# Kernel tuning notes

Measured on AMD Instinct MI355X. Metric: run time of the kernel, lower is better.

## Reference

```python
import jax, jax.numpy as jnp
import numpy as np

C = 32
KSHAPE = (C, C, 3, 3)  # (C_out, C_in, kH, kW)
BN_EPS = 1e-5


def _binary_act(x):
    # forward: sign(x); backward: identity clipped to |x|<1 (STE)
    xc = jnp.clip(x, -1.0, 1.0)
    return jax.lax.stop_gradient(jnp.sign(x) - xc) + xc


def _binarize_weight(w_flat, shape):
    w = w_flat.reshape(shape)
    scale = jax.lax.stop_gradient(jnp.mean(jnp.abs(w)))  # global scalar scale, detached
    wc = jnp.clip(w, -1.0, 1.0)
    # forward: scale*sign(w); backward flows through clamp(w,-1,1)
    return jax.lax.stop_gradient(scale * jnp.sign(w) - wc) + wc


def _bi_conv_bn(x, w_flat, gamma, beta, stride):
    xb = _binary_act(x)
    w = _binarize_weight(w_flat, KSHAPE)
    y = jax.lax.conv_general_dilated(
        xb, w, window_strides=(stride, stride), padding=[(1, 1), (1, 1)],
        dimension_numbers=('NCHW', 'OIHW', 'NCHW'))
    # BatchNorm2d in training mode (batch stats, biased variance)
    m = jnp.mean(y, axis=(0, 2, 3), keepdims=True)
    v = jnp.mean((y - m) ** 2, axis=(0, 2, 3), keepdims=True)
    yhat = (y - m) * jax.lax.rsqrt(v + BN_EPS)
    return gamma.reshape(1, -1, 1, 1) * yhat + beta.reshape(1, -1, 1, 1)


def setup_inputs() -> dict:
    key = jax.random.key(0)
    k1, k2, k3 = jax.random.split(key, 3)
    return {
        'x': jax.random.normal(k1, (32, C, 160, 160), dtype=jnp.float32),
        'w1': jax.random.normal(k2, (C * C * 9, 1), dtype=jnp.float32) * 0.05,
        'gamma1': jnp.ones((C,), dtype=jnp.float32),
        'beta1': jnp.zeros((C,), dtype=jnp.float32),
        'w2': jax.random.normal(k3, (C * C * 9, 1), dtype=jnp.float32) * 0.05,
        'gamma2': jnp.ones((C,), dtype=jnp.float32),
        'beta2': jnp.zeros((C,), dtype=jnp.float32),
    }


def reference(x, w1, gamma1, beta1, w2, gamma2, beta2):
    # bireal residual block, stride=1 => skip_op is Identity
    inner = _bi_conv_bn(x, w1, gamma1, beta1, 1) + x
    out = _bi_conv_bn(inner, w2, gamma2, beta2, 1) + inner
    return out
```

## Files before the change

### kernel.cpp

```cpp
#include <hip/hip_runtime.h>
#include <stdint.h>

#define NIMG 32
#define CH 32
#define HH 160
#define WW 160
#define HWL (HH*WW)
#define PRS 164
#define PHH 162
#define PIMG (PHH*PRS)
#define NPIX (NIMG*HWL)
#define HALO_WORDS 968

#define OFF_P     0
#define OFF_P2    3400704
#define OFF_IT    (OFF_P2 + 3400704)
#define OFF_WP    (OFF_IT + 52428800)
#define OFF_CORR  (OFF_WP + 2304)
#define OFF_SC    (OFF_CORR + 2304)
#define OFF_SB    (OFF_SC + 128)

struct StatLine {
  int s1; int pad0; unsigned long long s2; char pad[112];
};

#define AS1 __attribute__((address_space(1)))
#define AS3 __attribute__((address_space(3)))
__device__ __forceinline__ void dma16(const void* g, void* l) {
  __builtin_amdgcn_global_load_lds((const AS1 void*)g, (AS3 void*)l, 16, 0, 0);
}

__device__ __forceinline__ unsigned short f2bf(float f) {
  unsigned u = __float_as_uint(f);
  u += 0x7fffu + ((u >> 16) & 1u);
  return (unsigned short)(u >> 16);
}
__device__ __forceinline__ float bf2f(unsigned short u) {
  return __uint_as_float((uint32_t)u << 16);
}

__device__ __forceinline__ void conv4(const uint32_t r[3][6], const uint32_t* wsh,
                                      int co, int& a0, int& a1, int& a2, int& a3)
{
  a0 = a1 = a2 = a3 = 0;
  #pragma unroll
  for (int dy = 0; dy < 3; ++dy) {
    #pragma unroll
    for (int dx = 0; dx < 3; ++dx) {
      uint32_t wvv = wsh[co * 9 + dy * 3 + dx];
      a0 += __popc(r[dy][0 + dx] ^ wvv);
      a1 += __popc(r[dy][1 + dx] ^ wvv);
      a2 += __popc(r[dy][2 + dx] ^ wvv);
      a3 += __popc(r[dy][3 + dx] ^ wvv);
    }
  }
}

__device__ __forceinline__ void bn_affine(const float* SCp, const StatLine* sb,
    const float* gamma, const float* beta, int c, float& A, float& B)
{
  double sc = (double)SCp[0];
  double m  = sc * (double)sb[c].s1 / (double)NPIX;
  double ms = sc * sc * (double)(long long)sb[c].s2 / (double)NPIX;
  float inv = (float)(1.0 / sqrt(ms - m * m + 1e-5));
  float gm = gamma[c];
  A = gm * inv * (float)sc;
  B = beta[c] - gm * inv * (float)m;
}

__global__ __launch_bounds__(256) void pack_prep(const float* __restrict__ x,
    const float* __restrict__ w1, const float* __restrict__ w2,
    uint32_t* __restrict__ P, uint32_t* __restrict__ P2, uint32_t* __restrict__ WP,
    int* __restrict__ CORR, float* __restrict__ SC, StatLine* __restrict__ SB)
{
  __shared__ float lds[8192];
  const int tid = threadIdx.x;
  const int b = blockIdx.x;

  if (b >= 3200) {
    if (b == 3442) {
      int* z = (int*)SB;
      for (int i = tid; i < 2048; i += 256) z[i] = 0;
      float* red = lds;
      uint32_t* wpl = (uint32_t*)(lds + 256);
      for (int cv = 0; cv < 2; ++cv) {
        const float* w = cv ? w2 : w1;
        float s = 0.f;
        #pragma unroll
        for (int j = 0; j < 9; ++j) {
          float4 v = *reinterpret_cast<const float4*>(w + (j * 256 + tid) * 4);
          s += fabsf(v.x) + fabsf(v.y) + fabsf(v.z) + fabsf(v.w);
        }
        red[tid] = s;
        __syncthreads();
        for (int st = 128; st > 0; st >>= 1) {
          if (tid < st) red[tid] += red[tid + st];
          __syncthreads();
        }
        if (tid == 0) SC[cv] = red[0] / 9216.0f;
        for (int i = tid; i < 288; i += 256) {
          int co = i / 9, t = i - co * 9;
          uint32_t bw = 0;
          for (int ci = 0; ci < 32; ++ci)
            bw |= (w[(co * 32 + ci) * 9 + t] > 0.0f) ? (1u << ci) : 0u;
          WP[cv * 288 + i] = bw;
          wpl[i] = bw;
        }
        __syncthreads();
        for (int i = tid; i < 288; i += 256) {
          int cls = i / 32, co = i - cls * 32;
          int hc = cls / 3, wc = cls - hc * 3;
          int corr = 0;
          for (int t = 0; t < 9; ++t) {
            int dy = t / 3 - 1, dx = t % 3 - 1;
            bool inval = (hc == 0 && dy == -1) || (hc == 2 && dy == 1) ||
                         (wc == 0 && dx == -1) || (wc == 2 && dx == 1);
            if (inval) corr += 32 - 2 * __popc(wpl[co * 9 + t]);
          }
          CORR[cv * 288 + cls * 32 + co] = corr;
        }
        __syncthreads();
      }
    } else {
      int k = (b - 3200) * 256 + tid;
      uint32_t* buf = (k < 32 * HALO_WORDS) ? P : P2;
      int j = k % (32 * HALO_WORDS);
      int img = j / HALO_WORDS;
      int r = j - img * HALO_WORDS;
      int pr, pc;
      if (r < 164)      { pr = 0;   pc = r; }
      else if (r < 328) { pr = 161; pc = r - 164; }
      else {
        int k2 = r - 328;
        pr = 1 + (k2 >> 2);
        int q = k2 & 3;
        pc = (q == 0) ? 0 : (160 + q);
      }
      buf[img * PIMG + pr * PRS + pc] = 0;
    }
    return;
  }

  int n = b / 100;
  int p0 = (b - n * 100) * 256;
  const float* xb = x + (size_t)n * CH * HWL + p0;
  #pragma unroll
  for (int it = 0; it < 8; ++it) {
    int c = it * 4 + (tid >> 6);
    dma16(xb + (size_t)c * HWL + (tid & 63) * 4, lds + c * 256);
  }
  __syncthreads();

  uint32_t bits = 0;
  #pragma unroll
  for (int c = 0; c < 32; ++c) {
    if (lds[c * 256 + tid] > 0.f) bits |= 1u << c;
  }
  int px = p0 + tid;
  int h = px / WW, w = px - h * WW;
  P[n * PIMG + (h + 1) * PRS + (w + 1)] = bits;
}

__global__ __launch_bounds__(256) void conv_stats(const uint32_t* __restrict__ P,
    const uint32_t* __restrict__ WP, const int* __restrict__ CORR,
    StatLine* __restrict__ sb)
{
  __shared__ uint32_t wsh[288];
  __shared__ int csh[288];
  __shared__ int ls1[32], ls2[32];
  const int tid = threadIdx.x;
  for (int i = tid; i < 288; i += 256) { wsh[i] = WP[i]; csh[i] = CORR[i]; }
  if (tid < 32) { ls1[tid] = 0; ls2[tid] = 0; }
  __syncthreads();

  int g = blockIdx.x * 256 + tid;
  int w4 = g % 40;
  int t1 = g / 40;
  int h = t1 % 160;
  int n = t1 / 160;

  const uint32_t* base = P + n * PIMG + h * PRS + w4 * 4;
  uint32_t r[3][6];
  #pragma unroll
  for (int dy = 0; dy < 3; ++dy) {
    uint4 a = *reinterpret_cast<const uint4*>(base + dy * PRS);
    uint2 bw = *reinterpret_cast<const uint2*>(base + dy * PRS + 4);
    r[dy][0] = a.x; r[dy][1] = a.y; r[dy][2] = a.z; r[dy][3] = a.w;
    r[dy][4] = bw.x; r[dy][5] = bw.y;
  }

  int rowc = (h == 0) ? 0 : ((h == 159) ? 6 : 3);
  int cls0  = rowc + ((w4 == 0) ? 0 : 1);
  int cls12 = rowc + 1;
  int cls3  = rowc + ((w4 == 39) ? 2 : 1);
  int lane = tid & 63;

  #pragma unroll
  for (int co = 0; co < 32; ++co) {
    int a0, a1, a2, a3;
    conv4(r, wsh, co, a0, a1, a2, a3);
    int d0 = 288 - 2 * a0 - csh[cls0 * 32 + co];
    int d1 = 288 - 2 * a1 - csh[cls12 * 32 + co];
    int d2 = 288 - 2 * a2 - csh[cls12 * 32 + co];
    int d3 = 288 - 2 * a3 - csh[cls3 * 32 + co];
    int ds = d0 + d1 + d2 + d3;
    int sq = d0 * d0 + d1 * d1 + d2 * d2 + d3 * d3;
    #pragma unroll
    for (int off = 32; off > 0; off >>= 1) {
      ds += __shfl_down(ds, off);
      sq += __shfl_down(sq, off);
    }
    if (lane == 0) { atomicAdd(&ls1[co], ds); atomicAdd(&ls2[co], sq); }
  }
  __syncthreads();
  if (tid < 32) {
    atomicAdd(&sb[tid].s1, ls1[tid]);
    atomicAdd(&sb[tid].s2, (unsigned long long)(long long)ls2[tid]);
  }
}

__global__ __launch_bounds__(256) void conv_bn1(const uint32_t* __restrict__ P,
    const uint32_t* __restrict__ WP, const int* __restrict__ CORR,
    const float* __restrict__ x, const float* __restrict__ SCp,
    const StatLine* __restrict__ sb, const float* __restrict__ gamma,
    const float* __restrict__ beta, unsigned short* __restrict__ IT,
    uint32_t* __restrict__ P2)
{
  __shared__ float xs[8192];
  __shared__ uint32_t wsh[288];
  __shared__ int csh[288];
  __shared__ float Ash[32], Bsh[32];
  const int tid = threadIdx.x;
  const int b = blockIdx.x;
  int n = b / 100;
  int p0 = (b - n * 100) * 256;
  const float* xb = x + (size_t)n * CH * HWL + p0;

  #pragma unroll
  for (int it = 0; it < 8; ++it) {
    int c = it * 4 + (tid >> 6);
    dma16(xb + (size_t)c * HWL + (tid & 63) * 4, xs + c * 256);
  }

  for (int i = tid; i < 288; i += 256) { wsh[i] = WP[i]; csh[i] = CORR[i]; }
  if (tid < 32) bn_affine(SCp, sb, gamma, beta, tid, Ash[tid], Bsh[tid]);

  int px = p0 + tid;
  int h = px / WW, w = px - h * WW;
  const uint32_t* bp = P + n * PIMG + h * PRS + w;
  uint32_t r9[3][3];
  #pragma unroll
  for (int dy = 0; dy < 3; ++dy) {
    r9[dy][0] = bp[dy * PRS + 0];
    r9[dy][1] = bp[dy * PRS + 1];
    r9[dy][2] = bp[dy * PRS + 2];
  }
  int hc = (h == 0) ? 0 : ((h == 159) ? 2 : 1);
  int wc = (w == 0) ? 0 : ((w == 159) ? 2 : 1);
  int cls = hc * 3 + wc;

  __syncthreads();

  uint32_t bits = 0;
  uint32_t ow[16];
  #pragma unroll
  for (int co = 0; co < 32; ++co) {
    int a = 0;
    #pragma unroll
    for (int dy = 0; dy < 3; ++dy) {
      #pragma unroll
      for (int dx = 0; dx < 3; ++dx)
        a += __popc(r9[dy][dx] ^ wsh[co * 9 + dy * 3 + dx]);
    }
    int d = 288 - 2 * a - csh[cls * 32 + co];
    float v = fmaf(Ash[co], (float)d, Bsh[co]) + xs[co * 256 + tid];
    if (v > 0.f) bits |= 1u << co;
    uint32_t bf = (uint32_t)f2bf(v);
    if ((co & 1) == 0) ow[co >> 1] = bf;
    else               ow[co >> 1] |= bf << 16;
  }
  P2[n * PIMG + (h + 1) * PRS + (w + 1)] = bits;
  uint4* ip = (uint4*)(IT + (size_t)(n * HWL + px) * 32);
  ip[0] = make_uint4(ow[0], ow[1], ow[2], ow[3]);
  ip[1] = make_uint4(ow[4], ow[5], ow[6], ow[7]);
  ip[2] = make_uint4(ow[8], ow[9], ow[10], ow[11]);
  ip[3] = make_uint4(ow[12], ow[13], ow[14], ow[15]);
}

__global__ __launch_bounds__(256, 2) void conv_bn2(const uint32_t* __restrict__ P2,
    const uint32_t* __restrict__ WP, const int* __restrict__ CORR,
    const unsigned short* __restrict__ IT, const float* __restrict__ SCp,
    const StatLine* __restrict__ sb, const float* __restrict__ gamma,
    const float* __restrict__ beta, float* __restrict__ out)
{
  __shared__ uint32_t wsh[288];
  __shared__ int csh[288];
  __shared__ float Ash[32], Bsh[32];
  const int tid = threadIdx.x;
  for (int i = tid; i < 288; i += 256) { wsh[i] = WP[i]; csh[i] = CORR[i]; }
  if (tid < 32) bn_affine(SCp, sb, gamma, beta, tid, Ash[tid], Bsh[tid]);
  __syncthreads();

  int g = blockIdx.x * 256 + tid;
  int w4 = g % 40;
  int t1 = g / 40;
  int h = t1 % 160;
  int n = t1 / 160;

  const uint32_t* base = P2 + n * PIMG + h * PRS + w4 * 4;
  uint32_t r[3][6];
  #pragma unroll
  for (int dy = 0; dy < 3; ++dy) {
    uint4 a = *reinterpret_cast<const uint4*>(base + dy * PRS);
    uint2 bw = *reinterpret_cast<const uint2*>(base + dy * PRS + 4);
    r[dy][0] = a.x; r[dy][1] = a.y; r[dy][2] = a.z; r[dy][3] = a.w;
    r[dy][4] = bw.x; r[dy][5] = bw.y;
  }
  int rowc = (h == 0) ? 0 : ((h == 159) ? 6 : 3);
  int cls0  = rowc + ((w4 == 0) ? 0 : 1);
  int cls12 = rowc + 1;
  int cls3  = rowc + ((w4 == 39) ? 2 : 1);

  int i = h * WW + w4 * 4;
  size_t pbase = (size_t)n * CH * HWL + i;

  uint4 tt[16];
  const uint4* ip = (const uint4*)(IT + (size_t)(n * HWL + i) * 32);
  #pragma unroll
  for (int q = 0; q < 16; ++q) tt[q] = ip[q];

  #pragma unroll
  for (int co = 0; co < 32; ++co) {
    int e0, e1, e2, e3;
    conv4(r, wsh, co, e0, e1, e2, e3);
    int f0 = 288 - 2 * e0 - csh[cls0 * 32 + co];
    int f1 = 288 - 2 * e1 - csh[cls12 * 32 + co];
    int f2 = 288 - 2 * e2 - csh[cls12 * 32 + co];
    int f3 = 288 - 2 * e3 - csh[cls3 * 32 + co];
    float A = Ash[co], Bv = Bsh[co];
    const int qw = co >> 3;
    const int ws = (co >> 1) & 3;
    const int hf = co & 1;
    uint32_t u0 = (ws == 0) ? tt[0 * 4 + qw].x : (ws == 1) ? tt[0 * 4 + qw].y
                : (ws == 2) ? tt[0 * 4 + qw].z : tt[0 * 4 + qw].w;
    uint32_t u1 = (ws == 0) ? tt[1 * 4 + qw].x : (ws == 1) ? tt[1 * 4 + qw].y
                : (ws == 2) ? tt[1 * 4 + qw].z : tt[1 * 4 + qw].w;
    uint32_t u2 = (ws == 0) ? tt[2 * 4 + qw].x : (ws == 1) ? tt[2 * 4 + qw].y
                : (ws == 2) ? tt[2 * 4 + qw].z : tt[2 * 4 + qw].w;
    uint32_t u3 = (ws == 0) ? tt[3 * 4 + qw].x : (ws == 1) ? tt[3 * 4 + qw].y
                : (ws == 2) ? tt[3 * 4 + qw].z : tt[3 * 4 + qw].w;
    float i0 = bf2f((unsigned short)(hf ? (u0 >> 16) : (u0 & 0xffff)));
    float i1 = bf2f((unsigned short)(hf ? (u1 >> 16) : (u1 & 0xffff)));
    float i2 = bf2f((unsigned short)(hf ? (u2 >> 16) : (u2 & 0xffff)));
    float i3 = bf2f((unsigned short)(hf ? (u3 >> 16) : (u3 & 0xffff)));
    float4 o;
    o.x = fmaf(A, (float)f0, Bv) + i0;
    o.y = fmaf(A, (float)f1, Bv) + i1;
    o.z = fmaf(A, (float)f2, Bv) + i2;
    o.w = fmaf(A, (float)f3, Bv) + i3;
    *reinterpret_cast<float4*>(out + pbase + (size_t)co * HWL) = o;
  }
}

extern "C" void kernel_launch(void* const* d_in, const int* in_sizes, int n_in,
                              void* d_out, int out_size, void* d_ws, size_t ws_size,
                              hipStream_t stream)
{
  (void)in_sizes; (void)n_in; (void)out_size; (void)ws_size;
  const float* x  = (const float*)d_in[0];
  const float* w1 = (const float*)d_in[1];
  const float* g1 = (const float*)d_in[2];
  const float* b1 = (const float*)d_in[3];
  const float* w2 = (const float*)d_in[4];
  const float* g2 = (const float*)d_in[5];
  const float* b2 = (const float*)d_in[6];
  float* out = (float*)d_out;
  char* ws = (char*)d_ws;

  uint32_t*       P    = (uint32_t*)(ws + OFF_P);
  uint32_t*       P2   = (uint32_t*)(ws + OFF_P2);
  unsigned short* IT   = (unsigned short*)(ws + OFF_IT);
  uint32_t*       WP   = (uint32_t*)(ws + OFF_WP);
  int*            CORR = (int*)(ws + OFF_CORR);
  float*          SC   = (float*)(ws + OFF_SC);
  StatLine*       SB   = (StatLine*)(ws + OFF_SB);

  pack_prep<<<3443, 256, 0, stream>>>(x, w1, w2, P, P2, WP, CORR, SC, SB);
  conv_stats<<<800, 256, 0, stream>>>(P, WP, CORR, SB);
  conv_bn1<<<3200, 256, 0, stream>>>(P, WP, CORR, x, SC, SB, g1, b1, IT, P2);
  conv_stats<<<800, 256, 0, stream>>>(P2, WP + 288, CORR + 288, SB + 32);
  conv_bn2<<<800, 256, 0, stream>>>(P2, WP + 288, CORR + 288, IT, SC + 1, SB + 32, g2, b2, out);
}
```

Baseline: 201.5 us.

## Store bf16 intermediate planar NCHW and stage it through LDS in conv_bn2

The bf16 residual intermediate moves from pixel-major (NHWC, 64B per pixel) to channel-planar NCHW layout. conv_bn1 now processes two pixels per thread with 512-pixel blocks, loading x in two 16-channel halves into LDS and writing coalesced ushort2 per channel. conv_bn2 DMA-loads the planar intermediate tile into LDS and computes two pixels per thread instead of four, with coalesced float2 output writes. The aim is to remove strided, poorly coalesced accesses and register-heavy unpacking, at the cost of extra barriers and a 32KB LDS tile that may limit occupancy.

Result: faster. 181.1 us (-10.1%).

```diff
diff --git a/kernel.cpp b/kernel.cpp
--- a/kernel.cpp
+++ b/kernel.cpp
@@ -14,8 +14,8 @@
 
 #define OFF_P     0
 #define OFF_P2    3400704
-#define OFF_IT    (OFF_P2 + 3400704)
-#define OFF_WP    (OFF_IT + 52428800)
+#define OFF_IN    (OFF_P2 + 3400704)
+#define OFF_WP    (OFF_IN + 52428800)
 #define OFF_CORR  (OFF_WP + 2304)
 #define OFF_SC    (OFF_CORR + 2304)
 #define OFF_SB    (OFF_SC + 128)
@@ -52,6 +52,21 @@
       a1 += __popc(r[dy][1 + dx] ^ wvv);
       a2 += __popc(r[dy][2 + dx] ^ wvv);
       a3 += __popc(r[dy][3 + dx] ^ wvv);
+    }
+  }
+}
+
+__device__ __forceinline__ void conv2(const uint32_t r[3][4], const uint32_t* wsh,
+                                      int co, int& a0, int& a1)
+{
+  a0 = a1 = 0;
+  #pragma unroll
+  for (int dy = 0; dy < 3; ++dy) {
+    #pragma unroll
+    for (int dx = 0; dx < 3; ++dx) {
+      uint32_t wvv = wsh[co * 9 + dy * 3 + dx];
+      a0 += __popc(r[dy][dx] ^ wvv);
+      a1 += __popc(r[dy][dx + 1] ^ wvv);
     }
   }
 }
@@ -223,7 +238,7 @@
     const uint32_t* __restrict__ WP, const int* __restrict__ CORR,
     const float* __restrict__ x, const float* __restrict__ SCp,
     const StatLine* __restrict__ sb, const float* __restrict__ gamma,
-    const float* __restrict__ beta, unsigned short* __restrict__ IT,
+    const float* __restrict__ beta, unsigned short* __restrict__ IN,
     uint32_t* __restrict__ P2)
 {
   __shared__ float xs[8192];
@@ -232,133 +247,133 @@
   __shared__ float Ash[32], Bsh[32];
   const int tid = threadIdx.x;
   const int b = blockIdx.x;
-  int n = b / 100;
-  int p0 = (b - n * 100) * 256;
+  int n = b / 50;
+  int p0 = (b - n * 50) * 512;
   const float* xb = x + (size_t)n * CH * HWL + p0;
 
   #pragma unroll
   for (int it = 0; it < 8; ++it) {
-    int c = it * 4 + (tid >> 6);
-    dma16(xb + (size_t)c * HWL + (tid & 63) * 4, xs + c * 256);
-  }
-
+    int q = it * 4 + (tid >> 6);
+    int c = q >> 1, hf = q & 1;
+    dma16(xb + (size_t)c * HWL + hf * 256 + (tid & 63) * 4,
+          xs + c * 512 + hf * 256 + (tid & 63) * 4);
+  }
   for (int i = tid; i < 288; i += 256) { wsh[i] = WP[i]; csh[i] = CORR[i]; }
   if (tid < 32) bn_affine(SCp, sb, gamma, beta, tid, Ash[tid], Bsh[tid]);
 
-  int px = p0 + tid;
-  int h = px / WW, w = px - h * WW;
-  const uint32_t* bp = P + n * PIMG + h * PRS + w;
-  uint32_t r9[3][3];
+  int p = p0 + 2 * tid;
+  int h = p / WW, wloc = p - h * WW;
+  const uint32_t* bp = P + n * PIMG + h * PRS + wloc;
+  uint32_t r[3][4];
   #pragma unroll
   for (int dy = 0; dy < 3; ++dy) {
-    r9[dy][0] = bp[dy * PRS + 0];
-    r9[dy][1] = bp[dy * PRS + 1];
-    r9[dy][2] = bp[dy * PRS + 2];
-  }
-  int hc = (h == 0) ? 0 : ((h == 159) ? 2 : 1);
-  int wc = (w == 0) ? 0 : ((w == 159) ? 2 : 1);
-  int cls = hc * 3 + wc;
-
-  __syncthreads();
-
-  uint32_t bits = 0;
-  uint32_t ow[16];
-  #pragma unroll
-  for (int co = 0; co < 32; ++co) {
-    int a = 0;
-    #pragma unroll
-    for (int dy = 0; dy < 3; ++dy) {
-      #pragma unroll
-      for (int dx = 0; dx < 3; ++dx)
-        a += __popc(r9[dy][dx] ^ wsh[co * 9 + dy * 3 + dx]);
-    }
-    int d = 288 - 2 * a - csh[cls * 32 + co];
-    float v = fmaf(Ash[co], (float)d, Bsh[co]) + xs[co * 256 + tid];
-    if (v > 0.f) bits |= 1u << co;
-    uint32_t bf = (uint32_t)f2bf(v);
-    if ((co & 1) == 0) ow[co >> 1] = bf;
-    else               ow[co >> 1] |= bf << 16;
-  }
-  P2[n * PIMG + (h + 1) * PRS + (w + 1)] = bits;
-  uint4* ip = (uint4*)(IT + (size_t)(n * HWL + px) * 32);
-  ip[0] = make_uint4(ow[0], ow[1], ow[2], ow[3]);
-  ip[1] = make_uint4(ow[4], ow[5], ow[6], ow[7]);
-  ip[2] = make_uint4(ow[8], ow[9], ow[10], ow[11]);
-  ip[3] = make_uint4(ow[12], ow[13], ow[14], ow[15]);
-}
-
-__global__ __launch_bounds__(256, 2) void conv_bn2(const uint32_t* __restrict__ P2,
+    uint2 u0 = *reinterpret_cast<const uint2*>(bp + dy * PRS);
+    uint2 u1 = *reinterpret_cast<const uint2*>(bp + dy * PRS + 2);
+    r[dy][0] = u0.x; r[dy][1] = u0.y; r[dy][2] = u1.x; r[dy][3] = u1.y;
+  }
+  int rowc = (h == 0) ? 0 : ((h == 159) ? 6 : 3);
+  int cls0 = rowc + ((wloc == 0) ? 0 : 1);
+  int cls1 = rowc + ((wloc == 158) ? 2 : 1);
+  size_t ibase = (size_t)n * CH * HWL + p;
+
+  __syncthreads();
+
+  uint32_t bb0 = 0, bb1 = 0;
+  #pragma unroll
+  for (int co = 0; co < 16; ++co) {
+    int a0, a1;
+    conv2(r, wsh, co, a0, a1);
+    int d0 = 288 - 2 * a0 - csh[cls0 * 32 + co];
+    int d1 = 288 - 2 * a1 - csh[cls1 * 32 + co];
+    float2 xv = *reinterpret_cast<const float2*>(xs + co * 512 + 2 * tid);
+    float v0 = fmaf(Ash[co], (float)d0, Bsh[co]) + xv.x;
+    float v1 = fmaf(Ash[co], (float)d1, Bsh[co]) + xv.y;
+    ushort2 o; o.x = f2bf(v0); o.y = f2bf(v1);
+    *reinterpret_cast<ushort2*>(IN + ibase + (size_t)co * HWL) = o;
+    if (v0 > 0.f) bb0 |= 1u << co;
+    if (v1 > 0.f) bb1 |= 1u << co;
+  }
+  __syncthreads();
+
+  #pragma unroll
+  for (int it = 0; it < 8; ++it) {
+    int q = it * 4 + (tid >> 6);
+    int c = q >> 1, hf = q & 1;
+    dma16(xb + (size_t)(16 + c) * HWL + hf * 256 + (tid & 63) * 4,
+          xs + c * 512 + hf * 256 + (tid & 63) * 4);
+  }
+  __syncthreads();
+
+  #pragma unroll
+  for (int co = 16; co < 32; ++co) {
+    int a0, a1;
+    conv2(r, wsh, co, a0, a1);
+    int d0 = 288 - 2 * a0 - csh[cls0 * 32 + co];
+    int d1 = 288 - 2 * a1 - csh[cls1 * 32 + co];
+    float2 xv = *reinterpret_cast<const float2*>(xs + (co - 16) * 512 + 2 * tid);
+    float v0 = fmaf(Ash[co], (float)d0, Bsh[co]) + xv.x;
+    float v1 = fmaf(Ash[co], (float)d1, Bsh[co]) + xv.y;
+    ushort2 o; o.x = f2bf(v0); o.y = f2bf(v1);
+    *reinterpret_cast<ushort2*>(IN + ibase + (size_t)co * HWL) = o;
+    if (v0 > 0.f) bb0 |= 1u << co;
+    if (v1 > 0.f) bb1 |= 1u << co;
+  }
+  uint32_t* pw = P2 + n * PIMG + (h + 1) * PRS + (wloc + 1);
+  pw[0] = bb0; pw[1] = bb1;
+}
+
+__global__ __launch_bounds__(256) void conv_bn2(const uint32_t* __restrict__ P2,
     const uint32_t* __restrict__ WP, const int* __restrict__ CORR,
-    const unsigned short* __restrict__ IT, const float* __restrict__ SCp,
+    const unsigned short* __restrict__ IN, const float* __restrict__ SCp,
     const StatLine* __restrict__ sb, const float* __restrict__ gamma,
     const float* __restrict__ beta, float* __restrict__ out)
 {
+  __shared__ unsigned short is[16384];
   __shared__ uint32_t wsh[288];
   __shared__ int csh[288];
   __shared__ float Ash[32], Bsh[32];
   const int tid = threadIdx.x;
+  const int b = blockIdx.x;
+  int n = b / 50;
+  int p0 = (b - n * 50) * 512;
+  const unsigned short* ib = IN + (size_t)n * CH * HWL + p0;
+
+  #pragma unroll
+  for (int it = 0; it < 8; ++it) {
+    int c = it * 4 + (tid >> 6);
+    dma16(ib + (size_t)c * HWL + (tid & 63) * 8, is + c * 512 + (tid & 63) * 8);
+  }
   for (int i = tid; i < 288; i += 256) { wsh[i] = WP[i]; csh[i] = CORR[i]; }
   if (tid < 32) bn_affine(SCp, sb, gamma, beta, tid, Ash[tid], Bsh[tid]);
-  __syncthreads();
-
-  int g = blockIdx.x * 256 + tid;
-  int w4 = g % 40;
-  int t1 = g / 40;
-  int h = t1 % 160;
-  int n = t1 / 160;
-
-  const uint32_t* base = P2 + n * PIMG + h * PRS + w4 * 4;
-  uint32_t r[3][6];
+
+  int p = p0 + 2 * tid;
+  int h = p / WW, wloc = p - h * WW;
+  const uint32_t* bp = P2 + n * PIMG + h * PRS + wloc;
+  uint32_t r[3][4];
   #pragma unroll
   for (int dy = 0; dy < 3; ++dy) {
-    uint4 a = *reinterpret_cast<const uint4*>(base + dy * PRS);
-    uint2 bw = *reinterpret_cast<const uint2*>(base + dy * PRS + 4);
-    r[dy][0] = a.x; r[dy][1] = a.y; r[dy][2] = a.z; r[dy][3] = a.w;
-    r[dy][4] = bw.x; r[dy][5] = bw.y;
+    uint2 u0 = *reinterpret_cast<const uint2*>(bp + dy * PRS);
+    uint2 u1 = *reinterpret_cast<const uint2*>(bp + dy * PRS + 2);
+    r[dy][0] = u0.x; r[dy][1] = u0.y; r[dy][2] = u1.x; r[dy][3] = u1.y;
   }
   int rowc = (h == 0) ? 0 : ((h == 159) ? 6 : 3);
-  int cls0  = rowc + ((w4 == 0) ? 0 : 1);
-  int cls12 = rowc + 1;
-  int cls3  = rowc + ((w4 == 39) ? 2 : 1);
-
-  int i = h * WW + w4 * 4;
-  size_t pbase = (size_t)n * CH * HWL + i;
-
-  uint4 tt[16];
-  const uint4* ip = (const uint4*)(IT + (size_t)(n * HWL + i) * 32);
-  #pragma unroll
-  for (int q = 0; q < 16; ++q) tt[q] = ip[q];
+  int cls0 = rowc + ((wloc == 0) ? 0 : 1);
+  int cls1 = rowc + ((wloc == 158) ? 2 : 1);
+  size_t obase = (size_t)n * CH * HWL + p;
+
+  __syncthreads();
 
   #pragma unroll
   for (int co = 0; co < 32; ++co) {
-    int e0, e1, e2, e3;
-    conv4(r, wsh, co, e0, e1, e2, e3);
-    int f0 = 288 - 2 * e0 - csh[cls0 * 32 + co];
-    int f1 = 288 - 2 * e1 - csh[cls12 * 32 + co];
-    int f2 = 288 - 2 * e2 - csh[cls12 * 32 + co];
-    int f3 = 288 - 2 * e3 - csh[cls3 * 32 + co];
-    float A = Ash[co], Bv = Bsh[co];
-    const int qw = co >> 3;
-    const int ws = (co >> 1) & 3;
-    const int hf = co & 1;
-    uint32_t u0 = (ws == 0) ? tt[0 * 4 + qw].x : (ws == 1) ? tt[0 * 4 + qw].y
-                : (ws == 2) ? tt[0 * 4 + qw].z : tt[0 * 4 + qw].w;
-    uint32_t u1 = (ws == 0) ? tt[1 * 4 + qw].x : (ws == 1) ? tt[1 * 4 + qw].y
-                : (ws == 2) ? tt[1 * 4 + qw].z : tt[1 * 4 + qw].w;
-    uint32_t u2 = (ws == 0) ? tt[2 * 4 + qw].x : (ws == 1) ? tt[2 * 4 + qw].y
-                : (ws == 2) ? tt[2 * 4 + qw].z : tt[2 * 4 + qw].w;
-    uint32_t u3 = (ws == 0) ? tt[3 * 4 + qw].x : (ws == 1) ? tt[3 * 4 + qw].y
-                : (ws == 2) ? tt[3 * 4 + qw].z : tt[3 * 4 + qw].w;
-    float i0 = bf2f((unsigned short)(hf ? (u0 >> 16) : (u0 & 0xffff)));
-    float i1 = bf2f((unsigned short)(hf ? (u1 >> 16) : (u1 & 0xffff)));
-    float i2 = bf2f((unsigned short)(hf ? (u2 >> 16) : (u2 & 0xffff)));
-    float i3 = bf2f((unsigned short)(hf ? (u3 >> 16) : (u3 & 0xffff)));
-    float4 o;
-    o.x = fmaf(A, (float)f0, Bv) + i0;
-    o.y = fmaf(A, (float)f1, Bv) + i1;
-    o.z = fmaf(A, (float)f2, Bv) + i2;
-    o.w = fmaf(A, (float)f3, Bv) + i3;
-    *reinterpret_cast<float4*>(out + pbase + (size_t)co * HWL) = o;
+    int a0, a1;
+    conv2(r, wsh, co, a0, a1);
+    int f0 = 288 - 2 * a0 - csh[cls0 * 32 + co];
+    int f1 = 288 - 2 * a1 - csh[cls1 * 32 + co];
+    ushort2 iv = *reinterpret_cast<const ushort2*>(is + co * 512 + 2 * tid);
+    float2 o;
+    o.x = fmaf(Ash[co], (float)f0, Bsh[co]) + bf2f(iv.x);
+    o.y = fmaf(Ash[co], (float)f1, Bsh[co]) + bf2f(iv.y);
+    *reinterpret_cast<float2*>(out + obase + (size_t)co * HWL) = o;
   }
 }
 
@@ -379,7 +394,7 @@
 
   uint32_t*       P    = (uint32_t*)(ws + OFF_P);
   uint32_t*       P2   = (uint32_t*)(ws + OFF_P2);
-  unsigned short* IT   = (unsigned short*)(ws + OFF_IT);
+  unsigned short* IN   = (unsigned short*)(ws + OFF_IN);
   uint32_t*       WP   = (uint32_t*)(ws + OFF_WP);
   int*            CORR = (int*)(ws + OFF_CORR);
   float*          SC   = (float*)(ws + OFF_SC);
@@ -387,7 +402,7 @@
 
   pack_prep<<<3443, 256, 0, stream>>>(x, w1, w2, P, P2, WP, CORR, SC, SB);
   conv_stats<<<800, 256, 0, stream>>>(P, WP, CORR, SB);
-  conv_bn1<<<3200, 256, 0, stream>>>(P, WP, CORR, x, SC, SB, g1, b1, IT, P2);
+  conv_bn1<<<1600, 256, 0, stream>>>(P, WP, CORR, x, SC, SB, g1, b1, IN, P2);
   conv_stats<<<800, 256, 0, stream>>>(P2, WP + 288, CORR + 288, SB + 32);
-  conv_bn2<<<800, 256, 0, stream>>>(P2, WP + 288, CORR + 288, IT, SC + 1, SB + 32, g2, b2, out);
-}
+  conv_bn2<<<1600, 256, 0, stream>>>(P2, WP + 288, CORR + 288, IN, SC + 1, SB + 32, g2, b2, out);
+}
```
